# Performance work log

Hardware: AMD Instinct MI355X
Metric: run time of the kernel (lower is better)

Reference implementation:

```python
import jax, jax.numpy as jnp
import numpy as np

SIZE = 384  # output resolution
SCALE = (0.8, 1.0)


def _bilinear_crop_resize(img, cs, top, left):
    """img: [C,H,W]; cs/top/left: int32 scalars. Crop [top:top+cs, left:left+cs],
    resize to SIZE x SIZE with bilinear, align_corners=False (PyTorch semantics)."""
    csf = cs.astype(jnp.float32)
    # source coords within the crop, clamped like PyTorch (src = max(src,0), upper bounded)
    coords = (jnp.arange(SIZE, dtype=jnp.float32) + 0.5) * (csf / SIZE) - 0.5
    coords = jnp.clip(coords, 0.0, csf - 1.0)
    i0 = jnp.floor(coords).astype(jnp.int32)
    i1 = jnp.minimum(i0 + 1, cs - 1)
    w = coords - i0.astype(jnp.float32)  # [SIZE]
    y0, y1 = i0 + top, i1 + top
    x0, x1 = i0 + left, i1 + left
    wy, wx = w[:, None], w[None, :]
    g = lambda yy, xx: img[:, yy[:, None], xx[None, :]]  # [C,SIZE,SIZE]
    return (g(y0, x0) * (1 - wy) * (1 - wx)
            + g(y0, x1) * (1 - wy) * wx
            + g(y1, x0) * wy * (1 - wx)
            + g(y1, x1) * wy * wx)


def _nearest_crop_resize(msk, cs, top, left):
    """msk: [1,H,W]. PyTorch mode='nearest': src_idx = floor(dst * in/out)."""
    idx = jnp.floor(jnp.arange(SIZE, dtype=jnp.float32) * cs.astype(jnp.float32) / SIZE).astype(jnp.int32)
    idx = jnp.minimum(idx, cs - 1)
    y, x = idx + top, idx + left
    return msk[:, y[:, None], x[None, :]]


def setup_inputs() -> dict:
    key = jax.random.key(0)
    k1, k2, k3, k4, k5 = jax.random.split(key, 5)
    B, C, H, W = 32, 3, 512, 512
    image = jax.random.normal(k1, (B, C, H, W), dtype=jnp.float32)
    mask = (jax.random.uniform(k2, (B, 1, H, W)) > 0.5).astype(jnp.float32)
    scale = jax.random.uniform(k3, (B,), minval=SCALE[0], maxval=SCALE[1])
    crop_size = (scale * min(H, W)).astype(jnp.int32)
    max_y = (H - crop_size).astype(jnp.float32)
    max_x = (W - crop_size).astype(jnp.float32)
    top = jnp.where(max_y > 0, jnp.floor(jax.random.uniform(k4, (B,)) * max_y), 0.0).astype(jnp.int32)
    left = jnp.where(max_x > 0, jnp.floor(jax.random.uniform(k5, (B,)) * max_x), 0.0).astype(jnp.int32)
    return {"image": image, "mask": mask, "crop_size": crop_size, "top": top, "left": left}


def reference(image, mask, crop_size, top, left):
    img_out = jax.vmap(_bilinear_crop_resize)(image, crop_size, top, left)
    msk_out = jax.vmap(_nearest_crop_resize)(mask, crop_size, top, left)
    return img_out, msk_out
```

## Files before the change

kernel.cpp:

```cpp
#include <hip/hip_runtime.h>


constexpr int OUT = 384;
constexpr int H = 512;
constexpr int W = 512;
constexpr int B = 32;
constexpr int C = 3;
constexpr int NBLK = B * OUT;
constexpr int BPX  = NBLK / 8;

typedef float f32x4 __attribute__((ext_vector_type(4)));

__global__ __launch_bounds__(384) void rrc_pair_kernel(
    const float* __restrict__ image,
    const float* __restrict__ mask,
    const int* __restrict__ crop_size,
    const int* __restrict__ top,
    const int* __restrict__ left,
    float* __restrict__ img_out,
    float* __restrict__ msk_out)
{
    __shared__ float lds[2 * C][W];

    const int hw = blockIdx.x;
    const int logical = (hw & 7) * BPX + (hw >> 3);
    const int b = logical / OUT;
    const int i = logical % OUT;
    const int tid = (int)threadIdx.x;

    const int cs = crop_size[b];
    const int t  = top[b];
    const int l  = left[b];
    const float csf = (float)cs;
    const float s   = csf / (float)OUT;

    float cy = ((float)i + 0.5f) * s - 0.5f;
    cy = fminf(fmaxf(cy, 0.0f), csf - 1.0f);
    int   iy0 = (int)floorf(cy);
    int   iy1 = min(iy0 + 1, cs - 1);
    float wy  = cy - (float)iy0;
    const int y0 = iy0 + t, y1 = iy1 + t;

    const float* imgb = image + (size_t)b * C * H * W;

    {
        const int base = tid * 8;
        const int r    = base >> 9;
        const int col  = base & 511;
        const int c    = r >> 1;
        const int y    = (r & 1) ? y1 : y0;
        const float* src = imgb + ((size_t)c * H + (size_t)y) * W + col;
        f32x4 a0 = *(const f32x4*)src;
        f32x4 a1 = *(const f32x4*)(src + 4);
        *(f32x4*)&lds[r][col]     = a0;
        *(f32x4*)&lds[r][col + 4] = a1;
    }

    int my = (i * cs) / OUT;   my = min(my, cs - 1);
    int mx = (tid * cs) / OUT; mx = min(mx, cs - 1);
    const float mval = mask[((size_t)b * H + (size_t)(my + t)) * W + (mx + l)];

    __syncthreads();

    const int j = tid;
    float cx = ((float)j + 0.5f) * s - 0.5f;
    cx = fminf(fmaxf(cx, 0.0f), csf - 1.0f);
    int   ix0 = (int)floorf(cx);
    int   ix1 = min(ix0 + 1, cs - 1);
    float wx  = cx - (float)ix0;
    const int x0 = ix0 + l, x1 = ix1 + l;

    const float w00 = (1.0f - wy) * (1.0f - wx);
    const float w01 = (1.0f - wy) * wx;
    const float w10 = wy * (1.0f - wx);
    const float w11 = wy * wx;

    const size_t o_base = (size_t)b * C * OUT * OUT + (size_t)i * OUT + (size_t)j;

    #pragma unroll
    for (int c = 0; c < C; ++c) {
        float v00 = lds[c * 2][x0];
        float v01 = lds[c * 2][x1];
        float v10 = lds[c * 2 + 1][x0];
        float v11 = lds[c * 2 + 1][x1];
        float r = v00 * w00 + v01 * w01 + v10 * w10 + v11 * w11;
        __builtin_nontemporal_store(r, img_out + o_base + (size_t)c * OUT * OUT);
    }

    __builtin_nontemporal_store(mval,
        msk_out + (size_t)b * OUT * OUT + (size_t)i * OUT + (size_t)j);
}

extern "C" void kernel_launch(void* const* d_in, const int* in_sizes, int n_in,
                              void* d_out, int out_size, void* d_ws, size_t ws_size,
                              hipStream_t stream) {
    const float* image = (const float*)d_in[0];
    const float* mask  = (const float*)d_in[1];
    const int* cs      = (const int*)d_in[2];
    const int* top     = (const int*)d_in[3];
    const int* left    = (const int*)d_in[4];

    float* img_out = (float*)d_out;
    float* msk_out = img_out + (size_t)B * C * OUT * OUT;

    dim3 block(384);
    dim3 grid(NBLK);
    hipLaunchKernelGGL(rrc_pair_kernel, grid, block, 0, stream,
                       image, mask, cs, top, left, img_out, msk_out);
}
```

Measured before the change: 33.09 us.

## Process four output rows per block, sharing a six-row source window in LDS

Each block now produces four consecutive output rows instead of one. It loads a window of six source rows per channel into padded LDS and reuses them across the four rows. This cuts the number of blocks and the redundant global loads of overlapping source rows, since adjacent output rows share source rows. In exchange each block uses more LDS and does more work serially, and the x1 neighbour is read as x0+1 from a padded column rather than clamped explicitly.

```diff
diff --git a/kernel.cpp b/kernel.cpp
--- a/kernel.cpp
+++ b/kernel.cpp
@@ -6,12 +6,17 @@
 constexpr int W = 512;
 constexpr int B = 32;
 constexpr int C = 3;
-constexpr int NBLK = B * OUT;
+constexpr int RPB = 4;
+constexpr int GPB = OUT / RPB;
+constexpr int NBLK = B * GPB;
 constexpr int BPX  = NBLK / 8;
+constexpr int NSLOT = 6;
+constexpr int LROWS = C * NSLOT;
+constexpr int LDSW  = 520;
 
 typedef float f32x4 __attribute__((ext_vector_type(4)));
 
-__global__ __launch_bounds__(384) void rrc_pair_kernel(
+__global__ __launch_bounds__(OUT) void rrc_pair_kernel(
     const float* __restrict__ image,
     const float* __restrict__ mask,
     const int* __restrict__ crop_size,
@@ -20,12 +25,12 @@
     float* __restrict__ img_out,
     float* __restrict__ msk_out)
 {
-    __shared__ float lds[2 * C][W];
+    __shared__ float lds[LROWS * LDSW];
 
     const int hw = blockIdx.x;
     const int logical = (hw & 7) * BPX + (hw >> 3);
-    const int b = logical / OUT;
-    const int i = logical % OUT;
+    const int b  = logical / GPB;
+    const int i0 = (logical % GPB) * RPB;
     const int tid = (int)threadIdx.x;
 
     const int cs = crop_size[b];
@@ -34,61 +39,74 @@
     const float csf = (float)cs;
     const float s   = csf / (float)OUT;
 
-    float cy = ((float)i + 0.5f) * s - 0.5f;
-    cy = fminf(fmaxf(cy, 0.0f), csf - 1.0f);
-    int   iy0 = (int)floorf(cy);
-    int   iy1 = min(iy0 + 1, cs - 1);
-    float wy  = cy - (float)iy0;
-    const int y0 = iy0 + t, y1 = iy1 + t;
+    float cy0 = ((float)i0 + 0.5f) * s - 0.5f;
+    cy0 = fminf(fmaxf(cy0, 0.0f), csf - 1.0f);
+    const int base_y = (int)floorf(cy0);
 
     const float* imgb = image + (size_t)b * C * H * W;
 
-    {
-        const int base = tid * 8;
-        const int r    = base >> 9;
-        const int col  = base & 511;
-        const int c    = r >> 1;
-        const int y    = (r & 1) ? y1 : y0;
+    #pragma unroll
+    for (int k = 0; k < 6; ++k) {
+        const int q   = tid + k * OUT;
+        const int r   = q >> 7;
+        const int col = (q & 127) * 4;
+        const int c    = r / NSLOT;
+        const int slot = r % NSLOT;
+        const int y = min(t + base_y + slot, H - 1);
         const float* src = imgb + ((size_t)c * H + (size_t)y) * W + col;
-        f32x4 a0 = *(const f32x4*)src;
-        f32x4 a1 = *(const f32x4*)(src + 4);
-        *(f32x4*)&lds[r][col]     = a0;
-        *(f32x4*)&lds[r][col + 4] = a1;
+        f32x4 v = *(const f32x4*)src;
+        *(f32x4*)&lds[r * LDSW + col] = v;
+        if ((q & 127) == 127) lds[r * LDSW + 512] = v[3];
     }
 
-    int my = (i * cs) / OUT;   my = min(my, cs - 1);
-    int mx = (tid * cs) / OUT; mx = min(mx, cs - 1);
-    const float mval = mask[((size_t)b * H + (size_t)(my + t)) * W + (mx + l)];
+    float cx = ((float)tid + 0.5f) * s - 0.5f;
+    cx = fminf(fmaxf(cx, 0.0f), csf - 1.0f);
+    const int   ix0 = (int)floorf(cx);
+    const float wx  = cx - (float)ix0;
+    const int   x0  = ix0 + l;
+
+    const int mx = min((tid * cs) / OUT, cs - 1) + l;
+
+    float mval[RPB];
+    #pragma unroll
+    for (int r4 = 0; r4 < RPB; ++r4) {
+        const int i = i0 + r4;
+        int my = min((i * cs) / OUT, cs - 1);
+        mval[r4] = mask[((size_t)b * H + (size_t)(my + t)) * W + mx];
+    }
 
     __syncthreads();
 
-    const int j = tid;
-    float cx = ((float)j + 0.5f) * s - 0.5f;
-    cx = fminf(fmaxf(cx, 0.0f), csf - 1.0f);
-    int   ix0 = (int)floorf(cx);
-    int   ix1 = min(ix0 + 1, cs - 1);
-    float wx  = cx - (float)ix0;
-    const int x0 = ix0 + l, x1 = ix1 + l;
+    #pragma unroll
+    for (int r4 = 0; r4 < RPB; ++r4) {
+        const int i = i0 + r4;
+        float cy = ((float)i + 0.5f) * s - 0.5f;
+        cy = fminf(fmaxf(cy, 0.0f), csf - 1.0f);
+        int   iy0 = (int)floorf(cy);
+        int   iy1 = min(iy0 + 1, cs - 1);
+        float wy  = cy - (float)iy0;
+        const int slot0 = iy0 - base_y;
+        const int slot1 = min(iy1 - base_y, NSLOT - 1);
 
-    const float w00 = (1.0f - wy) * (1.0f - wx);
-    const float w01 = (1.0f - wy) * wx;
-    const float w10 = wy * (1.0f - wx);
-    const float w11 = wy * wx;
+        const float w00 = (1.0f - wy) * (1.0f - wx);
+        const float w01 = (1.0f - wy) * wx;
+        const float w10 = wy * (1.0f - wx);
+        const float w11 = wy * wx;
 
-    const size_t o_base = (size_t)b * C * OUT * OUT + (size_t)i * OUT + (size_t)j;
+        const size_t o_base = (size_t)b * C * OUT * OUT + (size_t)i * OUT + (size_t)tid;
 
-    #pragma unroll
-    for (int c = 0; c < C; ++c) {
-        float v00 = lds[c * 2][x0];
-        float v01 = lds[c * 2][x1];
-        float v10 = lds[c * 2 + 1][x0];
-        float v11 = lds[c * 2 + 1][x1];
-        float r = v00 * w00 + v01 * w01 + v10 * w10 + v11 * w11;
-        __builtin_nontemporal_store(r, img_out + o_base + (size_t)c * OUT * OUT);
+        #pragma unroll
+        for (int c = 0; c < C; ++c) {
+            const float* rA = &lds[(c * NSLOT + slot0) * LDSW + x0];
+            const float* rB = &lds[(c * NSLOT + slot1) * LDSW + x0];
+            float v00 = rA[0], v01 = rA[1];
+            float v10 = rB[0], v11 = rB[1];
+            float rr = v00 * w00 + v01 * w01 + v10 * w10 + v11 * w11;
+            __builtin_nontemporal_store(rr, img_out + o_base + (size_t)c * OUT * OUT);
+        }
+        __builtin_nontemporal_store(mval[r4],
+            msk_out + (size_t)b * OUT * OUT + (size_t)i * OUT + (size_t)tid);
     }
-
-    __builtin_nontemporal_store(mval,
-        msk_out + (size_t)b * OUT * OUT + (size_t)i * OUT + (size_t)j);
 }
 
 extern "C" void kernel_launch(void* const* d_in, const int* in_sizes, int n_in,
@@ -103,7 +121,7 @@
     float* img_out = (float*)d_out;
     float* msk_out = img_out + (size_t)B * C * OUT * OUT;
 
-    dim3 block(384);
+    dim3 block(OUT);
     dim3 grid(NBLK);
     hipLaunchKernelGGL(rrc_pair_kernel, grid, block, 0, stream,
                        image, mask, cs, top, left, img_out, msk_out);
```

After: 32.99 us. No clear change (-0.3%).
